# Performance work log

Hardware: AMD Instinct MI355X
Metric: run time of the kernel (lower is better)

The kernel has to match this reference:

```python
import jax, jax.numpy as jnp
import numpy as np

N_ITEMS = 100000
EMBED_DIM = 128
N_SESSIONS = 16384
TOTAL_ITEMS = 819200


def setup_inputs() -> dict:
    key = jax.random.key(0)
    k1, k2, k3 = jax.random.split(key, 3)
    embeddings = jax.random.normal(k1, (N_ITEMS, EMBED_DIM), dtype=jnp.float32)
    item_ids = jax.random.randint(k2, (TOTAL_ITEMS,), 0, N_ITEMS, dtype=jnp.int64)
    segment_ids = jnp.sort(jax.random.randint(k3, (TOTAL_ITEMS,), 0, N_SESSIONS, dtype=jnp.int64))
    return {"embeddings": embeddings, "item_ids": item_ids,
            "segment_ids": segment_ids, "num_sessions": N_SESSIONS}


def reference(embeddings, item_ids, segment_ids, num_sessions):
    # Ragged per-session mean of gathered item embeddings
    gathered = embeddings[item_ids]                      # [total_items, d]
    sums = jax.ops.segment_sum(gathered, segment_ids, num_segments=num_sessions)
    counts = jax.ops.segment_sum(jnp.ones((item_ids.shape[0],), dtype=embeddings.dtype),
                                 segment_ids, num_segments=num_sessions)
    counts = jnp.maximum(counts, 1.0)                    # guard empty sessions
    return sums / counts[:, None]                        # [num_sessions, d]
```

## Files before the change

kernel.cpp:

```cpp
#include <hip/hip_runtime.h>
#include <hip/hip_fp16.h>


constexpr int D = 128;
constexpr int IDS_CAP = 4096;

typedef float f32x2 __attribute__((ext_vector_type(2)));
typedef float f32x4 __attribute__((ext_vector_type(4)));
typedef unsigned int u32x2 __attribute__((ext_vector_type(2)));

__global__ __launch_bounds__(256)
void prep_kernel(const float* __restrict__ emb, __half* __restrict__ emb2,
                 const int* __restrict__ seg, int* __restrict__ starts,
                 int nitems, int total, int nsess, int repack_blocks) {
    if ((int)blockIdx.x < repack_blocks) {
        const int item = blockIdx.x * 4 + (threadIdx.x >> 6);
        if (item >= nitems) return;
        const int lane = threadIdx.x & 63;
        const f32x2 v = __builtin_nontemporal_load(
            reinterpret_cast<const f32x2*>(emb + (size_t)item * D) + lane);
        const __half2 h = __floats2half2_rn(v.x, v.y);
        const int g = lane >> 4;
        const int o = lane & 15;
        __half2* dst = reinterpret_cast<__half2*>(
            emb2 + (size_t)g * nitems * 32 + (size_t)item * 32);
        dst[o] = h;
    } else {
        const int j = ((int)blockIdx.x - repack_blocks) * 256 + threadIdx.x;
        if (j >= total) return;
        const int cur  = seg[j];
        const int prev = (j == 0) ? -1 : seg[j - 1];
        for (int s = prev + 1; s <= cur; ++s) starts[s] = j;
        if (j == total - 1) {
            for (int s = cur + 1; s <= nsess; ++s) starts[s] = total;
        }
    }
}

__global__ __launch_bounds__(256)
void gather_mean_g4(const __half* __restrict__ emb2,
                    const int* __restrict__ ids,
                    const int* __restrict__ starts,
                    float* __restrict__ out,
                    int nitems, int nsess) {
    __shared__ int lds_off[IDS_CAP];

    const int g    = blockIdx.x & 3;
    const int s0   = (blockIdx.x >> 2) * 32;
    const int sidx = s0 + (threadIdx.x >> 3);
    const int dl   = threadIdx.x & 7;

    const int sEnd  = (s0 + 32 < nsess) ? s0 + 32 : nsess;
    const int base0 = starts[s0];
    const int range = starts[sEnd] - base0;
    const bool use_lds = (range <= IDS_CAP);

    if (use_lds) {
        for (int t = threadIdx.x; t < range; t += 256)
            lds_off[t] = ids[base0 + t] << 6;
    }
    __syncthreads();

    if (sidx >= nsess) return;

    const int beg = starts[sidx];
    const int len = starts[sidx + 1] - beg;

    const char* pbase = reinterpret_cast<const char*>(emb2)
                      + (size_t)g * nitems * 64 + dl * 8;

    float a0 = 0.f, a1 = 0.f, a2 = 0.f, a3 = 0.f;

    if (use_lds) {
        const int* offp = lds_off + (beg - base0);
        int j = 0;
        for (; j + 8 <= len; j += 8) {
            int off[8];
            #pragma unroll
            for (int k = 0; k < 8; ++k) off[k] = offp[j + k];
            u32x2 r[8];
            #pragma unroll
            for (int k = 0; k < 8; ++k)
                r[k] = *reinterpret_cast<const u32x2*>(pbase + (size_t)off[k]);
            #pragma unroll
            for (int k = 0; k < 8; ++k) {
                unsigned lo = r[k].x, hi = r[k].y;
                const float2 f0 = __half22float2(*reinterpret_cast<const __half2*>(&lo));
                const float2 f1 = __half22float2(*reinterpret_cast<const __half2*>(&hi));
                a0 += f0.x; a1 += f0.y; a2 += f1.x; a3 += f1.y;
            }
        }
        for (; j < len; ++j) {
            const u32x2 r = *reinterpret_cast<const u32x2*>(pbase + (size_t)offp[j]);
            unsigned lo = r.x, hi = r.y;
            const float2 f0 = __half22float2(*reinterpret_cast<const __half2*>(&lo));
            const float2 f1 = __half22float2(*reinterpret_cast<const __half2*>(&hi));
            a0 += f0.x; a1 += f0.y; a2 += f1.x; a3 += f1.y;
        }
    } else {
        const int* idp = ids + beg;
        for (int j = 0; j < len; ++j) {
            const u32x2 r = *reinterpret_cast<const u32x2*>(
                pbase + ((size_t)idp[j] << 6));
            unsigned lo = r.x, hi = r.y;
            const float2 f0 = __half22float2(*reinterpret_cast<const __half2*>(&lo));
            const float2 f1 = __half22float2(*reinterpret_cast<const __half2*>(&hi));
            a0 += f0.x; a1 += f0.y; a2 += f1.x; a3 += f1.y;
        }
    }

    const float inv = (len > 0) ? 1.0f / (float)len : 0.0f;
    f32x4 o = {a0 * inv, a1 * inv, a2 * inv, a3 * inv};
    *reinterpret_cast<f32x4*>(out + (size_t)sidx * D + g * 32 + dl * 4) = o;
}

__global__ void find_starts_diff(const int* __restrict__ seg, int total,
                                 int nsess, int* __restrict__ starts) {
    int j = blockIdx.x * blockDim.x + threadIdx.x;
    if (j >= total) return;
    const int cur  = seg[j];
    const int prev = (j == 0) ? -1 : seg[j - 1];
    for (int s = prev + 1; s <= cur; ++s) starts[s] = j;
    if (j == total - 1) {
        for (int s = cur + 1; s <= nsess; ++s) starts[s] = total;
    }
}

__global__ __launch_bounds__(256)
void seg_mean_kernel(const float* __restrict__ emb,
                     const int* __restrict__ ids,
                     const int* __restrict__ starts,
                     float* __restrict__ out, int nsess) {
    const int tid  = threadIdx.x;
    const int s    = blockIdx.x * 4 + (tid >> 6);
    if (s >= nsess) return;
    const int lane = tid & 63;
    const int gq   = lane >> 5;
    const int l32  = lane & 31;

    const int beg = starts[s];
    const int end = starts[s + 1];

    float4 acc = make_float4(0.f, 0.f, 0.f, 0.f);
    for (int j = beg + gq; j < end; j += 2) {
        const int id = ids[j];
        const float4 v = reinterpret_cast<const float4*>(emb + (size_t)id * D)[l32];
        acc.x += v.x; acc.y += v.y; acc.z += v.z; acc.w += v.w;
    }
    acc.x += __shfl_down(acc.x, 32);
    acc.y += __shfl_down(acc.y, 32);
    acc.z += __shfl_down(acc.z, 32);
    acc.w += __shfl_down(acc.w, 32);
    if (lane < 32) {
        const int cnt = end - beg;
        const float inv = (cnt > 0) ? 1.0f / (float)cnt : 0.0f;
        const float4 o = make_float4(acc.x * inv, acc.y * inv,
                                     acc.z * inv, acc.w * inv);
        reinterpret_cast<float4*>(out + (size_t)s * D)[l32] = o;
    }
}

extern "C" void kernel_launch(void* const* d_in, const int* in_sizes, int n_in,
                              void* d_out, int out_size, void* d_ws, size_t ws_size,
                              hipStream_t stream) {
    const float* emb = (const float*)d_in[0];
    const int*   ids = (const int*)d_in[1];
    const int*   seg = (const int*)d_in[2];
    float*       out = (float*)d_out;

    const int total  = in_sizes[1];
    const int nsess  = out_size / D;
    const int nitems = in_sizes[0] / D;

    const size_t emb2_bytes = (size_t)nitems * D * 2;
    const size_t emb2_pad   = (emb2_bytes + 255) & ~(size_t)255;
    const size_t need       = emb2_pad + (size_t)(nsess + 1) * 4;

    if (ws_size >= need) {
        __half* emb2   = (__half*)d_ws;
        int*    starts = (int*)((char*)d_ws + emb2_pad);

        {
            const int repack_blocks = (nitems + 3) / 4;
            const int starts_blocks = (total + 255) / 256;
            prep_kernel<<<repack_blocks + starts_blocks, 256, 0, stream>>>(
                emb, emb2, seg, starts, nitems, total, nsess, repack_blocks);
        }
        {
            const int sgroups = (nsess + 31) / 32;
            gather_mean_g4<<<sgroups * 4, 256, 0, stream>>>(emb2, ids, starts,
                                                            out, nitems, nsess);
        }
    } else {
        int* starts = (int*)d_ws;
        {
            const int threads = 256;
            const int blocks = (total + threads - 1) / threads;
            find_starts_diff<<<blocks, threads, 0, stream>>>(seg, total, nsess, starts);
        }
        {
            const int blocks = (nsess + 3) / 4;
            seg_mean_kernel<<<blocks, 256, 0, stream>>>(emb, ids, starts, out, nsess);
        }
    }
}
```

Measured before the change: 54.32 us.

## Split gather by item-id halves with partial buffers and combine pass

```diff
diff --git a/kernel.cpp b/kernel.cpp
--- a/kernel.cpp
+++ b/kernel.cpp
@@ -38,6 +38,110 @@
 }
 
 __global__ __launch_bounds__(256)
+void gather_mean_half(const __half* __restrict__ emb2,
+                      const int* __restrict__ ids,
+                      const int* __restrict__ starts,
+                      float* __restrict__ partial,
+                      int nitems, int nsess) {
+    __shared__ int lds_off[IDS_CAP];
+
+    const int key  = blockIdx.x & 7;
+    const int g    = key & 3;
+    const int h    = key >> 2;
+    const int s0   = (blockIdx.x >> 3) * 32;
+    const int sidx = s0 + (threadIdx.x >> 3);
+    const int dl   = threadIdx.x & 7;
+
+    const int sEnd  = (s0 + 32 < nsess) ? s0 + 32 : nsess;
+    const int base0 = starts[s0];
+    const int range = starts[sEnd] - base0;
+    const bool use_lds = (range <= IDS_CAP);
+
+    if (use_lds) {
+        for (int t = threadIdx.x; t < range; t += 256)
+            lds_off[t] = ids[base0 + t] << 6;
+    }
+    __syncthreads();
+
+    if (sidx >= nsess) return;
+
+    const int beg = starts[sidx];
+    const int len = starts[sidx + 1] - beg;
+    const int hb  = (nitems >> 1) << 6;
+
+    const char* pbase = reinterpret_cast<const char*>(emb2)
+                      + (size_t)g * nitems * 64 + dl * 8;
+
+    float a0 = 0.f, a1 = 0.f, a2 = 0.f, a3 = 0.f;
+
+    if (use_lds) {
+        const int* offp = lds_off + (beg - base0);
+        int j = 0;
+        for (; j + 8 <= len; j += 8) {
+            u32x2 r[8];
+            #pragma unroll
+            for (int k = 0; k < 8; ++k) {
+                const int off = offp[j + k];
+                const bool take = h ? (off >= hb) : (off < hb);
+                r[k].x = 0u; r[k].y = 0u;
+                if (take)
+                    r[k] = *reinterpret_cast<const u32x2*>(pbase + (size_t)off);
+            }
+            #pragma unroll
+            for (int k = 0; k < 8; ++k) {
+                unsigned lo = r[k].x, hi = r[k].y;
+                const float2 f0 = __half22float2(*reinterpret_cast<const __half2*>(&lo));
+                const float2 f1 = __half22float2(*reinterpret_cast<const __half2*>(&hi));
+                a0 += f0.x; a1 += f0.y; a2 += f1.x; a3 += f1.y;
+            }
+        }
+        for (; j < len; ++j) {
+            const int off = offp[j];
+            const bool take = h ? (off >= hb) : (off < hb);
+            if (take) {
+                const u32x2 r = *reinterpret_cast<const u32x2*>(pbase + (size_t)off);
+                unsigned lo = r.x, hi = r.y;
+                const float2 f0 = __half22float2(*reinterpret_cast<const __half2*>(&lo));
+                const float2 f1 = __half22float2(*reinterpret_cast<const __half2*>(&hi));
+                a0 += f0.x; a1 += f0.y; a2 += f1.x; a3 += f1.y;
+            }
+        }
+    } else {
+        const int* idp = ids + beg;
+        for (int j = 0; j < len; ++j) {
+            const int off = idp[j] << 6;
+            const bool take = h ? (off >= hb) : (off < hb);
+            if (take) {
+                const u32x2 r = *reinterpret_cast<const u32x2*>(pbase + (size_t)off);
+                unsigned lo = r.x, hi = r.y;
+                const float2 f0 = __half22float2(*reinterpret_cast<const __half2*>(&lo));
+                const float2 f1 = __half22float2(*reinterpret_cast<const __half2*>(&hi));
+                a0 += f0.x; a1 += f0.y; a2 += f1.x; a3 += f1.y;
+            }
+        }
+    }
+
+    const float inv = (len > 0) ? 1.0f / (float)len : 0.0f;
+    f32x4 o = {a0 * inv, a1 * inv, a2 * inv, a3 * inv};
+    float* dst = partial + (size_t)h * nsess * D + (size_t)sidx * D
+               + g * 32 + dl * 4;
+    __builtin_nontemporal_store(o, reinterpret_cast<f32x4*>(dst));
+}
+
+__global__ __launch_bounds__(256)
+void combine_kernel(const float* __restrict__ partial, float* __restrict__ out,
+                    int n4) {
+    const int i = blockIdx.x * 256 + threadIdx.x;
+    if (i >= n4) return;
+    const f32x4 a = __builtin_nontemporal_load(
+        reinterpret_cast<const f32x4*>(partial) + i);
+    const f32x4 b = __builtin_nontemporal_load(
+        reinterpret_cast<const f32x4*>(partial) + n4 + i);
+    f32x4 o = {a.x + b.x, a.y + b.y, a.z + b.z, a.w + b.w};
+    reinterpret_cast<f32x4*>(out)[i] = o;
+}
+
+__global__ __launch_bounds__(256)
 void gather_mean_g4(const __half* __restrict__ emb2,
                     const int* __restrict__ ids,
                     const int* __restrict__ starts,
@@ -172,35 +276,47 @@
     const int nsess  = out_size / D;
     const int nitems = in_sizes[0] / D;
 
-    const size_t emb2_bytes = (size_t)nitems * D * 2;
-    const size_t emb2_pad   = (emb2_bytes + 255) & ~(size_t)255;
-    const size_t need       = emb2_pad + (size_t)(nsess + 1) * 4;
-
-    if (ws_size >= need) {
+    const size_t emb2_bytes   = (size_t)nitems * D * 2;
+    const size_t emb2_pad     = (emb2_bytes + 255) & ~(size_t)255;
+    const size_t starts_bytes = (size_t)(nsess + 1) * 4;
+    const size_t starts_pad   = (starts_bytes + 255) & ~(size_t)255;
+    const size_t partial_bytes = (size_t)2 * nsess * D * 4;
+    const size_t need_full = emb2_pad + starts_pad + partial_bytes;
+    const size_t need_mid  = emb2_pad + starts_bytes;
+
+    if (ws_size >= need_full) {
+        __half* emb2    = (__half*)d_ws;
+        int*    starts  = (int*)((char*)d_ws + emb2_pad);
+        float*  partial = (float*)((char*)d_ws + emb2_pad + starts_pad);
+
+        const int repack_blocks = (nitems + 3) / 4;
+        const int starts_blocks = (total + 255) / 256;
+        prep_kernel<<<repack_blocks + starts_blocks, 256, 0, stream>>>(
+            emb, emb2, seg, starts, nitems, total, nsess, repack_blocks);
+
+        const int sgroups = (nsess + 31) / 32;
+        gather_mean_half<<<sgroups * 8, 256, 0, stream>>>(emb2, ids, starts,
+                                                          partial, nitems, nsess);
+
+        const int n4 = nsess * (D / 4);
+        combine_kernel<<<(n4 + 255) / 256, 256, 0, stream>>>(partial, out, n4);
+    } else if (ws_size >= need_mid) {
         __half* emb2   = (__half*)d_ws;
         int*    starts = (int*)((char*)d_ws + emb2_pad);
 
-        {
-            const int repack_blocks = (nitems + 3) / 4;
-            const int starts_blocks = (total + 255) / 256;
-            prep_kernel<<<repack_blocks + starts_blocks, 256, 0, stream>>>(
-                emb, emb2, seg, starts, nitems, total, nsess, repack_blocks);
-        }
-        {
-            const int sgroups = (nsess + 31) / 32;
-            gather_mean_g4<<<sgroups * 4, 256, 0, stream>>>(emb2, ids, starts,
-                                                            out, nitems, nsess);
-        }
+        const int repack_blocks = (nitems + 3) / 4;
+        const int starts_blocks = (total + 255) / 256;
+        prep_kernel<<<repack_blocks + starts_blocks, 256, 0, stream>>>(
+            emb, emb2, seg, starts, nitems, total, nsess, repack_blocks);
+
+        const int sgroups = (nsess + 31) / 32;
+        gather_mean_g4<<<sgroups * 4, 256, 0, stream>>>(emb2, ids, starts,
+                                                        out, nitems, nsess);
     } else {
         int* starts = (int*)d_ws;
-        {
-            const int threads = 256;
-            const int blocks = (total + threads - 1) / threads;
-            find_starts_diff<<<blocks, threads, 0, stream>>>(seg, total, nsess, starts);
-        }
-        {
-            const int blocks = (nsess + 3) / 4;
-            seg_mean_kernel<<<blocks, 256, 0, stream>>>(emb, ids, starts, out, nsess);
-        }
-    }
-}
+        const int blocks = (total + 255) / 256;
+        find_starts_diff<<<blocks, 256, 0, stream>>>(seg, total, nsess, starts);
+        const int sblocks = (nsess + 3) / 4;
+        seg_mean_kernel<<<sblocks, 256, 0, stream>>>(emb, ids, starts, out, nsess);
+    }
+}
```

New measurement: 65.95 us. 21.4% more time.
